# Kernel tuning notes

Measured on AMD Instinct MI355X. Metric: run time of the kernel, lower is better.

## Reference

```python
import jax, jax.numpy as jnp
import numpy as np

B, L, E = 4, 2048, 1024
H, DQ, DV = 8, 128, 128
SCALE = 1.0 / np.sqrt(DQ).astype(np.float32)


def setup_inputs() -> dict:
    key = jax.random.key(0)
    ks = jax.random.split(key, 6)
    return {
        "qInputs": jax.random.normal(ks[0], (B, L, E), dtype=jnp.float32),
        "kvInputs": jax.random.normal(ks[1], (B, L, E), dtype=jnp.float32),
        "mask": jnp.zeros((B, H, L, L), dtype=jnp.bool_),
        "W_Q": jax.random.normal(ks[2], (E, H * DQ), dtype=jnp.float32) * 0.02,
        "W_K": jax.random.normal(ks[3], (E, H * DQ), dtype=jnp.float32) * 0.02,
        "W_V": jax.random.normal(ks[4], (E, H * DV), dtype=jnp.float32) * 0.02,
        "W_fc": jax.random.normal(ks[5], (H * DV, E), dtype=jnp.float32) * 0.02,
    }


def reference(qInputs, kvInputs, mask, W_Q, W_K, W_V, W_fc):
    b, lq, _ = qInputs.shape
    lk = kvInputs.shape[1]
    # Projections -> [B, H, L, D]
    Q = (qInputs @ W_Q).reshape(b, lq, H, DQ).transpose(0, 2, 1, 3)
    K = (kvInputs @ W_K).reshape(b, lk, H, DQ).transpose(0, 2, 1, 3)
    V = (kvInputs @ W_V).reshape(b, lk, H, DV).transpose(0, 2, 1, 3)
    # Scaled dot-product with additive mask fill of -1e9
    scores = jnp.einsum("bhqd,bhkd->bhqk", Q, K) * SCALE
    scores = jnp.where(mask, jnp.float32(-1e9), scores)
    attn = jax.nn.softmax(scores, axis=-1)
    ctx = jnp.einsum("bhqk,bhkd->bhqd", attn, V)
    ctx = ctx.transpose(0, 2, 1, 3).reshape(b, lq, H * DV)
    return ctx @ W_fc
```

## Files before the change

### kernel.cpp

```cpp
#include <hip/hip_runtime.h>
#include <stdint.h>

#define LQ 2048
#define EDIM 1024
#define HN 8
#define DH 128
#define BATCH 4
#define SCALE_LOG2E 0.12753785051263942f

typedef short bf16x8 __attribute__((ext_vector_type(8)));
typedef float f32x4 __attribute__((ext_vector_type(4)));
typedef unsigned short u16;
typedef unsigned short u16x4 __attribute__((ext_vector_type(4)));

__device__ __forceinline__ u16 f2bf(float f) {
  union { float f; uint32_t u; } c; c.f = f;
  uint32_t u = c.u;
  return (u16)((u + 0x7fffu + ((u >> 16) & 1u)) >> 16);
}

__device__ __forceinline__ void async16(const void* g, void* l) {
  __builtin_amdgcn_global_load_lds((const __attribute__((address_space(1))) void*)g,
                                   (__attribute__((address_space(3))) void*)l, 16, 0, 0);
}

__global__ __launch_bounds__(256) void prep_kernel(const float* __restrict__ qIn, const float* __restrict__ kvIn,
                                                   const float* __restrict__ w0, const float* __restrict__ w1,
                                                   const float* __restrict__ w2, const float* __restrict__ w3,
                                                   const unsigned char* __restrict__ mask,
                                                   u16* __restrict__ oq, u16* __restrict__ okv,
                                                   u16* __restrict__ o0, u16* __restrict__ o1,
                                                   u16* __restrict__ o2, u16* __restrict__ o3,
                                                   unsigned char* __restrict__ flags) {
  __shared__ float tile[32][33];
  __shared__ int wany[4];
  const int bid = blockIdx.x;
  const int t = threadIdx.x;
  if (bid < 16384) {
    const float* in = (bid >= 8192) ? kvIn : qIn;
    u16* out = (bid >= 8192) ? okv : oq;
    size_t i = (size_t)(bid & 8191) * 256 + t;
    float4 v = ((const float4*)in)[i];
    u16x4 o;
    o.x = f2bf(v.x); o.y = f2bf(v.y); o.z = f2bf(v.z); o.w = f2bf(v.w);
    ((u16x4*)out)[i] = o;
  } else if (bid < 20480) {
    const int idx = bid - 16384;
    const int z = idx >> 10;
    const int rem = idx & 1023;
    const float* in; u16* out;
    switch (z) {
      case 0: in = w0; out = o0; break;
      case 1: in = w1; out = o1; break;
      case 2: in = w2; out = o2; break;
      default: in = w3; out = o3; break;
    }
    const int tx = t & 31, ty = t >> 5;
    const int x0 = (rem & 31) * 32;
    const int y0 = (rem >> 5) * 32;
#pragma unroll
    for (int j = 0; j < 32; j += 8)
      tile[ty + j][tx] = in[(size_t)(y0 + ty + j) * EDIM + x0 + tx];
    __syncthreads();
#pragma unroll
    for (int j = 0; j < 32; j += 8)
      out[(size_t)(x0 + ty + j) * EDIM + (y0 + tx)] = f2bf(tile[tx][ty + j]);
  } else {
    const int idx = bid - 20480;
    const int bh = idx >> 8;
    const int tile16 = idx & 255;
    const int qt = tile16 >> 4, kt = tile16 & 15;
    const int r = t >> 1;
    const size_t base = ((size_t)bh * LQ + qt * 128 + r) * LQ + kt * 128 + (t & 1) * 64;
    const uint4* p = (const uint4*)(mask + base);
    uint4 a = p[0], c = p[1], d = p[2], e = p[3];
    uint32_t any = a.x | a.y | a.z | a.w | c.x | c.y | c.z | c.w |
                   d.x | d.y | d.z | d.w | e.x | e.y | e.z | e.w;
    int wa = __any(any != 0);
    if ((t & 63) == 0) wany[t >> 6] = wa;
    __syncthreads();
    if (t == 0)
      flags[(size_t)bh * 256 + tile16] = (unsigned char)(wany[0] | wany[1] | wany[2] | wany[3]);
  }
}

struct GemmCore {
  template <typename EpiF>
  static __device__ __forceinline__ void run(const u16* __restrict__ A, const u16* __restrict__ Bt,
                                             int m0, int n0, u16* As, u16* Bs, EpiF epi) {
    const int tid = threadIdx.x;
    const int l = tid & 63;
    const int w = tid >> 6;
    const int wm = (w >> 1) * 64;
    const int wn = (w & 1) * 64;
    const int fm = l & 15;
    const int q4 = l >> 4;
    const int f7 = fm & 7;
    f32x4 acc[4][4] = {};
    for (int k0 = 0; k0 < EDIM; k0 += 64) {
      __syncthreads();
#pragma unroll
      for (int ii = 0; ii < 4; ++ii) {
        const int rloc = w * 32 + ii * 8 + (l >> 3);
        const int cs = (l & 7) ^ (rloc & 7);
        async16(A + (size_t)(m0 + rloc) * EDIM + k0 + cs * 8, &As[(w * 32 + ii * 8) * 64 + l * 8]);
        async16(Bt + (size_t)(n0 + rloc) * EDIM + k0 + cs * 8, &Bs[(w * 32 + ii * 8) * 64 + l * 8]);
      }
      __syncthreads();
#pragma unroll
      for (int ks = 0; ks < 2; ++ks) {
        const int coff = ((ks * 4 + q4) ^ f7) * 8;
        bf16x8 a[4], b[4];
#pragma unroll
        for (int i = 0; i < 4; ++i) a[i] = *(const bf16x8*)&As[(wm + i * 16 + fm) * 64 + coff];
#pragma unroll
        for (int j = 0; j < 4; ++j) b[j] = *(const bf16x8*)&Bs[(wn + j * 16 + fm) * 64 + coff];
#pragma unroll
        for (int i = 0; i < 4; ++i)
#pragma unroll
          for (int j = 0; j < 4; ++j)
            acc[i][j] = __builtin_amdgcn_mfma_f32_16x16x32_bf16(a[i], b[j], acc[i][j], 0, 0, 0);
      }
    }
    const int rr = q4 * 4;
#pragma unroll
    for (int i = 0; i < 4; ++i)
#pragma unroll
      for (int j = 0; j < 4; ++j)
#pragma unroll
        for (int r = 0; r < 4; ++r)
          epi(m0 + wm + i * 16 + rr + r, n0 + wn + j * 16 + fm, acc[i][j][r]);
  }
};

__global__ __launch_bounds__(256) void qkv_gemm(const u16* __restrict__ xq, const u16* __restrict__ xkv,
                                                const u16* __restrict__ WqT, const u16* __restrict__ WkT,
                                                const u16* __restrict__ WvT,
                                                u16* __restrict__ Qb, u16* __restrict__ Kb,
                                                u16* __restrict__ Vt) {
  __shared__ __align__(16) u16 As[128 * 64];
  __shared__ __align__(16) u16 Bs[128 * 64];
  const int z = blockIdx.z;
  if (z == 0) {
    GemmCore::run(xq, WqT, blockIdx.x * 128, blockIdx.y * 128, As, Bs,
                  [&](int gm, int gn, float v) { Qb[(size_t)gm * EDIM + gn] = f2bf(v); });
  } else if (z == 1) {
    GemmCore::run(xkv, WkT, blockIdx.x * 128, blockIdx.y * 128, As, Bs,
                  [&](int gm, int gn, float v) { Kb[(size_t)gm * EDIM + gn] = f2bf(v); });
  } else {
    GemmCore::run(WvT, xkv, blockIdx.y * 128, blockIdx.x * 128, As, Bs,
                  [&](int gm, int gn, float v) {
                    Vt[((size_t)(gn >> 11) * 1024 + gm) * 2048 + (gn & 2047)] = f2bf(v);
                  });
  }
}

__global__ __launch_bounds__(256) void out_gemm(const u16* __restrict__ ctx, const u16* __restrict__ WfcT,
                                                float* __restrict__ out) {
  __shared__ __align__(16) u16 As[128 * 64];
  __shared__ __align__(16) u16 Bs[128 * 64];
  GemmCore::run(ctx, WfcT, blockIdx.x * 128, blockIdx.y * 128, As, Bs,
                [&](int gm, int gn, float v) { out[(size_t)gm * EDIM + gn] = v; });
}

__global__ __launch_bounds__(256, 2) void attn_kernel(const u16* __restrict__ Qb, const u16* __restrict__ Kb,
                                                      const u16* __restrict__ Vt,
                                                      const unsigned char* __restrict__ mask,
                                                      const unsigned char* __restrict__ flags,
                                                      u16* __restrict__ ctx) {
  __shared__ __align__(16) u16 KV[128 * 128];
  __shared__ __align__(16) u16 P[128 * 136];
  const int tid = threadIdx.x;
  const int l = tid & 63;
  const int w = tid >> 6;
  const int qt = blockIdx.x;
  const int h = blockIdx.y;
  const int b = blockIdx.z;
  const int fm = l & 15;
  const int q4 = l >> 4;
  const int fk = q4 * 8;
  const int swz = fm & 7;
  const int qbase = qt * 128 + w * 32;

  const unsigned char* tileFlags = flags + (size_t)(b * HN + h) * 256 + qt * 16;

  bf16x8 qf[2][4];
#pragma unroll
  for (int mt = 0; mt < 2; ++mt)
#pragma unroll
    for (int ks = 0; ks < 4; ++ks)
      qf[mt][ks] = *(const bf16x8*)(Qb + (size_t)(b * LQ + qbase + mt * 16 + fm) * EDIM + h * DH + ks * 32 + fk);

  f32x4 o[2][8] = {};
  float lsum[2][4] = {};

  const size_t mbase = (size_t)(b * HN + h) * (size_t)LQ * LQ;

  for (int kt = 0; kt < 16; ++kt) {
    __syncthreads();
#pragma unroll
    for (int ii = 0; ii < 8; ++ii) {
      int rloc = w * 32 + ii * 4 + q4;
      int cs = fm ^ (rloc & 7);
      async16(Kb + (size_t)(b * LQ + kt * 128 + rloc) * EDIM + h * DH + cs * 8,
              &KV[(w * 32 + ii * 4) * 128 + l * 8]);
    }
    __syncthreads();

    f32x4 s[2][8] = {};
#pragma unroll
    for (int ks = 0; ks < 4; ++ks) {
      const int koff = ((ks * 4 + q4) ^ swz) * 8;
#pragma unroll
      for (int nt = 0; nt < 8; ++nt) {
        bf16x8 kf = *(const bf16x8*)&KV[(nt * 16 + fm) * 128 + koff];
        s[0][nt] = __builtin_amdgcn_mfma_f32_16x16x32_bf16(qf[0][ks], kf, s[0][nt], 0, 0, 0);
        s[1][nt] = __builtin_amdgcn_mfma_f32_16x16x32_bf16(qf[1][ks], kf, s[1][nt], 0, 0, 0);
      }
    }
    __syncthreads();

#pragma unroll
    for (int ii = 0; ii < 8; ++ii) {
      int dloc = w * 32 + ii * 4 + q4;
      int cs = fm ^ (dloc & 7);
      async16(Vt + ((size_t)(b * HN + h) * DH + dloc) * LQ + kt * 128 + cs * 8,
              &KV[(w * 32 + ii * 4) * 128 + l * 8]);
    }

    const int hasMask = tileFlags[kt];
#pragma unroll
    for (int mt = 0; mt < 2; ++mt)
#pragma unroll
      for (int r = 0; r < 4; ++r) {
        float sum = 0.f;
        if (hasMask) {
          const int qr = qbase + mt * 16 + q4 * 4 + r;
          const unsigned char* mrow = mask + mbase + (size_t)qr * LQ + kt * 128 + fm;
#pragma unroll
          for (int nt = 0; nt < 8; ++nt) {
            float e = mrow[nt * 16] ? 0.f : exp2f(s[mt][nt][r] * SCALE_LOG2E);
            s[mt][nt][r] = e;
            sum += e;
          }
        } else {
#pragma unroll
          for (int nt = 0; nt < 8; ++nt) {
            float e = exp2f(s[mt][nt][r] * SCALE_LOG2E);
            s[mt][nt][r] = e;
            sum += e;
          }
        }
#pragma unroll
        for (int off = 1; off < 16; off <<= 1) sum += __shfl_xor(sum, off);
        lsum[mt][r] += sum;
      }
#pragma unroll
    for (int mt = 0; mt < 2; ++mt)
#pragma unroll
      for (int r = 0; r < 4; ++r)
#pragma unroll
        for (int nt = 0; nt < 8; ++nt)
          P[(w * 32 + mt * 16 + q4 * 4 + r) * 136 + nt * 16 + fm] = f2bf(s[mt][nt][r]);
    __syncthreads();

#pragma unroll
    for (int ns = 0; ns < 4; ++ns) {
      const int voff = ((ns * 4 + q4) ^ swz) * 8;
      bf16x8 pf0 = *(const bf16x8*)&P[(w * 32 + fm) * 136 + ns * 32 + fk];
      bf16x8 pf1 = *(const bf16x8*)&P[(w * 32 + 16 + fm) * 136 + ns * 32 + fk];
#pragma unroll
      for (int dt = 0; dt < 8; ++dt) {
        bf16x8 vf = *(const bf16x8*)&KV[(dt * 16 + fm) * 128 + voff];
        o[0][dt] = __builtin_amdgcn_mfma_f32_16x16x32_bf16(pf0, vf, o[0][dt], 0, 0, 0);
        o[1][dt] = __builtin_amdgcn_mfma_f32_16x16x32_bf16(pf1, vf, o[1][dt], 0, 0, 0);
      }
    }
  }
#pragma unroll
  for (int mt = 0; mt < 2; ++mt)
#pragma unroll
    for (int r = 0; r < 4; ++r) {
      float inv = 1.f / lsum[mt][r];
      int gq = b * LQ + qbase + mt * 16 + q4 * 4 + r;
#pragma unroll
      for (int dt = 0; dt < 8; ++dt)
        ctx[(size_t)gq * EDIM + h * DH + dt * 16 + fm] = f2bf(o[mt][dt][r] * inv);
    }
}

extern "C" void kernel_launch(void* const* d_in, const int* in_sizes, int n_in,
                              void* d_out, int out_size, void* d_ws, size_t ws_size,
                              hipStream_t stream) {
  const float* qIn = (const float*)d_in[0];
  const float* kvIn = (const float*)d_in[1];
  const unsigned char* mask = (const unsigned char*)d_in[2];
  const float* W_Q = (const float*)d_in[3];
  const float* W_K = (const float*)d_in[4];
  const float* W_V = (const float*)d_in[5];
  const float* W_fc = (const float*)d_in[6];
  float* out = (float*)d_out;

  uint8_t* ws = (uint8_t*)d_ws;
  const size_t MB = 1u << 20;
  u16* xq   = (u16*)(ws);
  u16* xkv  = (u16*)(ws + 16 * MB);
  u16* WqT  = (u16*)(ws + 32 * MB);
  u16* WkT  = (u16*)(ws + 34 * MB);
  u16* WvT  = (u16*)(ws + 36 * MB);
  u16* WfcT = (u16*)(ws + 38 * MB);
  u16* Qb   = (u16*)(ws + 40 * MB);
  u16* Kb   = (u16*)(ws + 56 * MB);
  u16* Vt   = (u16*)(ws + 72 * MB);
  u16* ctx  = (u16*)(ws + 88 * MB);
  unsigned char* flags = (unsigned char*)(ws + 104 * MB);

  prep_kernel<<<28672, 256, 0, stream>>>(qIn, kvIn, W_Q, W_K, W_V, W_fc, mask,
                                         xq, xkv, WqT, WkT, WvT, WfcT, flags);
  qkv_gemm<<<dim3(64, 8, 3), 256, 0, stream>>>(xq, xkv, WqT, WkT, WvT, Qb, Kb, Vt);
  attn_kernel<<<dim3(16, 8, 4), 256, 0, stream>>>(Qb, Kb, Vt, mask, flags, ctx);
  out_gemm<<<dim3(64, 8), 256, 0, stream>>>(ctx, WfcT, out);
}
```

Before: 895.9 us.

## Double-buffer K/V tiles with 64-key steps and per-wave P buffers in attention

Splits the key loop into 32 steps of 64 keys and double-buffers K and V tiles so the next tile's async loads overlap the current tile's MFMA work. P is now stored in a per-wave swizzled buffer, so the block-wide barriers around the P write and read go away. LDS reads are batched through inline asm, and mask flags are preloaded into a bitmask. The risks are that inline asm hides dependencies from the compiler, that barrier-only synchronisation of the async loads may be fragile, and that LDS use is higher.

```diff
diff --git a/kernel.cpp b/kernel.cpp
--- a/kernel.cpp
+++ b/kernel.cpp
@@ -22,6 +22,32 @@
 __device__ __forceinline__ void async16(const void* g, void* l) {
   __builtin_amdgcn_global_load_lds((const __attribute__((address_space(1))) void*)g,
                                    (__attribute__((address_space(3))) void*)l, 16, 0, 0);
+}
+
+__device__ __forceinline__ uint32_t lds_b(const u16* p) {
+  return (uint32_t)(uintptr_t)(__attribute__((address_space(3))) const u16*)p;
+}
+__device__ __forceinline__ void ldsr4(bf16x8& d0, bf16x8& d1, bf16x8& d2, bf16x8& d3,
+                                      uint32_t a0, uint32_t a1, uint32_t a2, uint32_t a3) {
+  asm volatile("ds_read_b128 %0, %4\n\t"
+               "ds_read_b128 %1, %5\n\t"
+               "ds_read_b128 %2, %6\n\t"
+               "ds_read_b128 %3, %7\n\t"
+               "s_waitcnt lgkmcnt(0)"
+               : "=&v"(d0), "=&v"(d1), "=&v"(d2), "=&v"(d3)
+               : "v"(a0), "v"(a1), "v"(a2), "v"(a3));
+}
+__device__ __forceinline__ void ldsr2(bf16x8& d0, bf16x8& d1, uint32_t a0, uint32_t a1) {
+  asm volatile("ds_read_b128 %0, %2\n\t"
+               "ds_read_b128 %1, %3\n\t"
+               "s_waitcnt lgkmcnt(0)"
+               : "=&v"(d0), "=&v"(d1) : "v"(a0), "v"(a1));
+}
+__device__ __forceinline__ void ldsw16(uint32_t a, u16 v) {
+  asm volatile("ds_write_b16 %0, %1" :: "v"(a), "v"((uint32_t)v));
+}
+__device__ __forceinline__ void lgkm_drain() {
+  asm volatile("s_waitcnt lgkmcnt(0)" ::: "memory");
 }
 
 __global__ __launch_bounds__(256) void prep_kernel(const float* __restrict__ qIn, const float* __restrict__ kvIn,
@@ -168,8 +194,9 @@
                                                       const unsigned char* __restrict__ mask,
                                                       const unsigned char* __restrict__ flags,
                                                       u16* __restrict__ ctx) {
-  __shared__ __align__(16) u16 KV[128 * 128];
-  __shared__ __align__(16) u16 P[128 * 136];
+  __shared__ __align__(16) u16 Ktile[2][64 * 128];
+  __shared__ __align__(16) u16 Vtile[2][128 * 64];
+  __shared__ __align__(16) u16 P[4 * 32 * 64];
   const int tid = threadIdx.x;
   const int l = tid & 63;
   const int w = tid >> 6;
@@ -179,10 +206,19 @@
   const int fm = l & 15;
   const int q4 = l >> 4;
   const int fk = q4 * 8;
-  const int swz = fm & 7;
+  const int f7 = fm & 7;
   const int qbase = qt * 128 + w * 32;
-
-  const unsigned char* tileFlags = flags + (size_t)(b * HN + h) * 256 + qt * 16;
+  const int bh = b * HN + h;
+  u16* Pw = &P[w * 2048];
+
+  const u16* Kbh = Kb + (size_t)b * LQ * EDIM + h * DH;
+  const u16* Vth = Vt + (size_t)bh * DH * LQ;
+  const size_t mbase = (size_t)bh * (size_t)LQ * LQ;
+
+  const unsigned char* tf = flags + (size_t)bh * 256 + qt * 16;
+  uint32_t fmask = 0;
+#pragma unroll
+  for (int i = 0; i < 16; ++i) fmask |= (tf[i] ? 1u : 0u) << i;
 
   bf16x8 qf[2][4];
 #pragma unroll
@@ -191,44 +227,59 @@
     for (int ks = 0; ks < 4; ++ks)
       qf[mt][ks] = *(const bf16x8*)(Qb + (size_t)(b * LQ + qbase + mt * 16 + fm) * EDIM + h * DH + ks * 32 + fk);
 
+  auto stageK = [&](int kt_, int buf) {
+#pragma unroll
+    for (int ii = 0; ii < 4; ++ii) {
+      const int i = w * 4 + ii;
+      const int row = i * 4 + (l >> 4);
+      const int g = (l & 15) ^ (row & 7);
+      async16(Kbh + (size_t)(kt_ * 64 + row) * EDIM + g * 8, &Ktile[buf][i * 512 + l * 8]);
+    }
+  };
+  auto stageV = [&](int kt_, int buf) {
+#pragma unroll
+    for (int ii = 0; ii < 4; ++ii) {
+      const int i = w * 4 + ii;
+      const int row = i * 8 + (l >> 3);
+      const int g = (l & 7) ^ (row & 7);
+      async16(Vth + (size_t)row * LQ + kt_ * 64 + g * 8, &Vtile[buf][i * 512 + l * 8]);
+    }
+  };
+
+  stageK(0, 0);
+  stageV(0, 0);
+
   f32x4 o[2][8] = {};
   float lsum[2][4] = {};
 
-  const size_t mbase = (size_t)(b * HN + h) * (size_t)LQ * LQ;
-
-  for (int kt = 0; kt < 16; ++kt) {
+  for (int kt = 0; kt < 32; ++kt) {
+    const int cur = kt & 1;
     __syncthreads();
-#pragma unroll
-    for (int ii = 0; ii < 8; ++ii) {
-      int rloc = w * 32 + ii * 4 + q4;
-      int cs = fm ^ (rloc & 7);
-      async16(Kb + (size_t)(b * LQ + kt * 128 + rloc) * EDIM + h * DH + cs * 8,
-              &KV[(w * 32 + ii * 4) * 128 + l * 8]);
-    }
-    __syncthreads();
-
-    f32x4 s[2][8] = {};
+    if (kt + 1 < 32) { stageK(kt + 1, 1 - cur); stageV(kt + 1, 1 - cur); }
+
+    const u16* KT = &Ktile[cur][0];
+    const u16* VT = &Vtile[cur][0];
+
+    f32x4 s[2][4] = {};
 #pragma unroll
     for (int ks = 0; ks < 4; ++ks) {
-      const int koff = ((ks * 4 + q4) ^ swz) * 8;
-#pragma unroll
-      for (int nt = 0; nt < 8; ++nt) {
-        bf16x8 kf = *(const bf16x8*)&KV[(nt * 16 + fm) * 128 + koff];
-        s[0][nt] = __builtin_amdgcn_mfma_f32_16x16x32_bf16(qf[0][ks], kf, s[0][nt], 0, 0, 0);
-        s[1][nt] = __builtin_amdgcn_mfma_f32_16x16x32_bf16(qf[1][ks], kf, s[1][nt], 0, 0, 0);
-      }
-    }
-    __syncthreads();
-
-#pragma unroll
-    for (int ii = 0; ii < 8; ++ii) {
-      int dloc = w * 32 + ii * 4 + q4;
-      int cs = fm ^ (dloc & 7);
-      async16(Vt + ((size_t)(b * HN + h) * DH + dloc) * LQ + kt * 128 + cs * 8,
-              &KV[(w * 32 + ii * 4) * 128 + l * 8]);
-    }
-
-    const int hasMask = tileFlags[kt];
+      const int slot = (ks * 4 + q4) ^ f7;
+      bf16x8 kf0, kf1, kf2, kf3;
+      ldsr4(kf0, kf1, kf2, kf3,
+            lds_b(KT + (0 * 16 + fm) * 128 + slot * 8),
+            lds_b(KT + (1 * 16 + fm) * 128 + slot * 8),
+            lds_b(KT + (2 * 16 + fm) * 128 + slot * 8),
+            lds_b(KT + (3 * 16 + fm) * 128 + slot * 8));
+#pragma unroll
+      for (int mt = 0; mt < 2; ++mt) {
+        s[mt][0] = __builtin_amdgcn_mfma_f32_16x16x32_bf16(qf[mt][ks], kf0, s[mt][0], 0, 0, 0);
+        s[mt][1] = __builtin_amdgcn_mfma_f32_16x16x32_bf16(qf[mt][ks], kf1, s[mt][1], 0, 0, 0);
+        s[mt][2] = __builtin_amdgcn_mfma_f32_16x16x32_bf16(qf[mt][ks], kf2, s[mt][2], 0, 0, 0);
+        s[mt][3] = __builtin_amdgcn_mfma_f32_16x16x32_bf16(qf[mt][ks], kf3, s[mt][3], 0, 0, 0);
+      }
+    }
+
+    const int hasMask = (fmask >> (kt >> 1)) & 1;
 #pragma unroll
     for (int mt = 0; mt < 2; ++mt)
 #pragma unroll
@@ -236,16 +287,16 @@
         float sum = 0.f;
         if (hasMask) {
           const int qr = qbase + mt * 16 + q4 * 4 + r;
-          const unsigned char* mrow = mask + mbase + (size_t)qr * LQ + kt * 128 + fm;
-#pragma unroll
-          for (int nt = 0; nt < 8; ++nt) {
+          const unsigned char* mrow = mask + mbase + (size_t)qr * LQ + kt * 64 + fm;
+#pragma unroll
+          for (int nt = 0; nt < 4; ++nt) {
             float e = mrow[nt * 16] ? 0.f : exp2f(s[mt][nt][r] * SCALE_LOG2E);
             s[mt][nt][r] = e;
             sum += e;
           }
         } else {
 #pragma unroll
-          for (int nt = 0; nt < 8; ++nt) {
+          for (int nt = 0; nt < 4; ++nt) {
             float e = exp2f(s[mt][nt][r] * SCALE_LOG2E);
             s[mt][nt][r] = e;
             sum += e;
@@ -255,28 +306,53 @@
         for (int off = 1; off < 16; off <<= 1) sum += __shfl_xor(sum, off);
         lsum[mt][r] += sum;
       }
+
 #pragma unroll
     for (int mt = 0; mt < 2; ++mt)
 #pragma unroll
-      for (int r = 0; r < 4; ++r)
-#pragma unroll
-        for (int nt = 0; nt < 8; ++nt)
-          P[(w * 32 + mt * 16 + q4 * 4 + r) * 136 + nt * 16 + fm] = f2bf(s[mt][nt][r]);
-    __syncthreads();
-
-#pragma unroll
-    for (int ns = 0; ns < 4; ++ns) {
-      const int voff = ((ns * 4 + q4) ^ swz) * 8;
-      bf16x8 pf0 = *(const bf16x8*)&P[(w * 32 + fm) * 136 + ns * 32 + fk];
-      bf16x8 pf1 = *(const bf16x8*)&P[(w * 32 + 16 + fm) * 136 + ns * 32 + fk];
-#pragma unroll
-      for (int dt = 0; dt < 8; ++dt) {
-        bf16x8 vf = *(const bf16x8*)&KV[(dt * 16 + fm) * 128 + voff];
-        o[0][dt] = __builtin_amdgcn_mfma_f32_16x16x32_bf16(pf0, vf, o[0][dt], 0, 0, 0);
-        o[1][dt] = __builtin_amdgcn_mfma_f32_16x16x32_bf16(pf1, vf, o[1][dt], 0, 0, 0);
-      }
+      for (int r = 0; r < 4; ++r) {
+        const int ql = mt * 16 + q4 * 4 + r;
+#pragma unroll
+        for (int nt = 0; nt < 4; ++nt) {
+          const int chunk = 2 * nt + (fm >> 3);
+          const int slot = chunk ^ (ql & 7);
+          ldsw16(lds_b(Pw + ql * 64 + slot * 8 + (fm & 7)), f2bf(s[mt][nt][r]));
+        }
+      }
+    lgkm_drain();
+
+#pragma unroll
+    for (int ns = 0; ns < 2; ++ns) {
+      const int pslot = (4 * ns + q4) ^ f7;
+      bf16x8 pf0, pf1;
+      ldsr2(pf0, pf1, lds_b(Pw + fm * 64 + pslot * 8), lds_b(Pw + (16 + fm) * 64 + pslot * 8));
+      const int vslot = (4 * ns + q4) ^ f7;
+      bf16x8 v0, v1, v2, v3, v4, v5, v6, v7;
+      ldsr4(v0, v1, v2, v3,
+            lds_b(VT + (0 * 16 + fm) * 64 + vslot * 8), lds_b(VT + (1 * 16 + fm) * 64 + vslot * 8),
+            lds_b(VT + (2 * 16 + fm) * 64 + vslot * 8), lds_b(VT + (3 * 16 + fm) * 64 + vslot * 8));
+      ldsr4(v4, v5, v6, v7,
+            lds_b(VT + (4 * 16 + fm) * 64 + vslot * 8), lds_b(VT + (5 * 16 + fm) * 64 + vslot * 8),
+            lds_b(VT + (6 * 16 + fm) * 64 + vslot * 8), lds_b(VT + (7 * 16 + fm) * 64 + vslot * 8));
+      o[0][0] = __builtin_amdgcn_mfma_f32_16x16x32_bf16(pf0, v0, o[0][0], 0, 0, 0);
+      o[1][0] = __builtin_amdgcn_mfma_f32_16x16x32_bf16(pf1, v0, o[1][0], 0, 0, 0);
+      o[0][1] = __builtin_amdgcn_mfma_f32_16x16x32_bf16(pf0, v1, o[0][1], 0, 0, 0);
+      o[1][1] = __builtin_amdgcn_mfma_f32_16x16x32_bf16(pf1, v1, o[1][1], 0, 0, 0);
+      o[0][2] = __builtin_amdgcn_mfma_f32_16x16x32_bf16(pf0, v2, o[0][2], 0, 0, 0);
+      o[1][2] = __builtin_amdgcn_mfma_f32_16x16x32_bf16(pf1, v2, o[1][2], 0, 0, 0);
+      o[0][3] = __builtin_amdgcn_mfma_f32_16x16x32_bf16(pf0, v3, o[0][3], 0, 0, 0);
+      o[1][3] = __builtin_amdgcn_mfma_f32_16x16x32_bf16(pf1, v3, o[1][3], 0, 0, 0);
+      o[0][4] = __builtin_amdgcn_mfma_f32_16x16x32_bf16(pf0, v4, o[0][4], 0, 0, 0);
+      o[1][4] = __builtin_amdgcn_mfma_f32_16x16x32_bf16(pf1, v4, o[1][4], 0, 0, 0);
+      o[0][5] = __builtin_amdgcn_mfma_f32_16x16x32_bf16(pf0, v5, o[0][5], 0, 0, 0);
+      o[1][5] = __builtin_amdgcn_mfma_f32_16x16x32_bf16(pf1, v5, o[1][5], 0, 0, 0);
+      o[0][6] = __builtin_amdgcn_mfma_f32_16x16x32_bf16(pf0, v6, o[0][6], 0, 0, 0);
+      o[1][6] = __builtin_amdgcn_mfma_f32_16x16x32_bf16(pf1, v6, o[1][6], 0, 0, 0);
+      o[0][7] = __builtin_amdgcn_mfma_f32_16x16x32_bf16(pf0, v7, o[0][7], 0, 0, 0);
+      o[1][7] = __builtin_amdgcn_mfma_f32_16x16x32_bf16(pf1, v7, o[1][7], 0, 0, 0);
     }
   }
+
 #pragma unroll
   for (int mt = 0; mt < 2; ++mt)
 #pragma unroll
```

Result: no change. 882.9 us (-1.5%).
